# Performance work log

Measured on AMD Instinct MI355X. Metric: run time of the kernel, lower is better.

Reference implementation:

```python
import jax, jax.numpy as jnp
import numpy as np

N_NODES = 50000
N_EDGES = 800000
N_GRAPHS = 64
IN_DIM = 128
HID = 256
N_LAYERS = 4
N_PROT = 5
N_CLASSES = 1
EPS = 1e-12


def setup_inputs() -> dict:
    key = jax.random.key(0)
    ks = jax.random.split(key, 10)
    h = jax.random.normal(ks[0], (N_NODES, IN_DIM), jnp.float32)
    src = jax.random.randint(ks[1], (N_EDGES,), 0, N_NODES, dtype=jnp.int32)
    dst = jax.random.randint(ks[2], (N_EDGES,), 0, N_NODES, dtype=jnp.int32)
    graph_id = jnp.sort(jax.random.randint(ks[3], (N_NODES,), 0, N_GRAPHS, dtype=jnp.int32))
    W_emb = jax.random.normal(ks[4], (IN_DIM, HID), jnp.float32) * 0.05
    b_emb = jnp.zeros((HID,), jnp.float32)
    Ws = jax.random.normal(ks[5], (N_LAYERS, 2 * HID, HID), jnp.float32) * 0.05
    bs = jnp.zeros((N_LAYERS, HID), jnp.float32)
    p_pos = jax.random.uniform(ks[6], (N_PROT, HID), jnp.float32)
    p_neg = jax.random.uniform(ks[7], (N_PROT, HID), jnp.float32)
    W_fc = jax.random.normal(ks[8], (N_CLASSES, 2 * N_PROT), jnp.float32) * 0.1
    return dict(h=h, src=src, dst=dst, graph_id=graph_id, W_emb=W_emb,
                b_emb=b_emb, Ws=Ws, bs=bs, p_pos=p_pos, p_neg=p_neg, W_fc=W_fc)


def _segment_mean(x, seg, num):
    # sum over segments, divide by count (empty segments -> 0, like DGL mean)
    s = jax.ops.segment_sum(x, seg, num_segments=num)
    cnt = jax.ops.segment_sum(jnp.ones((x.shape[0],), x.dtype), seg, num_segments=num)
    return s / jnp.maximum(cnt, 1.0)[:, None]


def _forward(h, src, dst, graph_id, W_emb, b_emb, Ws, bs, p_pos, p_neg, W_fc):
    x = h @ W_emb + b_emb  # [N, HID]
    for l in range(N_LAYERS):
        # mean aggregation of neighbor messages (copy_src -> mean at dst)
        c = _segment_mean(x[src], dst, N_NODES)  # [N, HID]
        bundle = jnp.concatenate([x, c], axis=1) @ Ws[l] + bs[l]  # [N, HID]
        # F.normalize(p=2, dim=1) then relu activation, then residual add
        norm = jnp.linalg.norm(bundle, axis=1, keepdims=True)
        bundle = bundle / jnp.maximum(norm, EPS)
        x = x + jax.nn.relu(bundle)
    hg = _segment_mean(x, graph_id, N_GRAPHS)  # dgl.mean_nodes -> [G, HID]

    def sims(P):
        d = jnp.sum((hg[:, None, :] - P[None, :, :]) ** 2, axis=-1)  # [G, P]
        return jnp.log((d + 1.0) / (d + EPS))

    ss = jnp.concatenate([sims(p_pos), sims(p_neg)], axis=1)  # [G, 2P]
    y = ss @ W_fc.T  # [G, n_classes]
    return jax.nn.sigmoid(y).squeeze()


def reference(h, src, dst, graph_id, W_emb, b_emb, Ws, bs, p_pos, p_neg, W_fc):
    return _forward(h, src, dst, graph_id, W_emb, b_emb, Ws, bs, p_pos, p_neg, W_fc)
```

## Files before the change

kernel.cpp:

```cpp
#include <hip/hip_runtime.h>
#include <math.h>

#define N_NODESC 50000
#define NPAD 50048
#define N_EDGESC 800000
#define N_GRAPHSC 64
#define IN_DIMC 128
#define HIDC 256
#define N_LAYERSC 4
#define EPSV 1e-12f

#define NBUCK 196
#define EPB 4096
#define NBLK1 196
#define WCONV_BLKS 2176
#define PBUCK 8192
#define ZROW 50000

typedef __attribute__((ext_vector_type(8))) short short8;
typedef __attribute__((ext_vector_type(4))) float floatx4;
typedef __attribute__((ext_vector_type(2))) float floatx2;

__device__ __forceinline__ unsigned short f2b(float f) {
    union { float f; unsigned u; } v; v.f = f;
    unsigned r = v.u + 0x7FFFu + ((v.u >> 16) & 1u);
    return (unsigned short)(r >> 16);
}
__device__ __forceinline__ unsigned pkb(float a, float b) {
    return (unsigned)f2b(a) | ((unsigned)f2b(b) << 16);
}
__device__ __forceinline__ unsigned char f2q(float v) {
    return (unsigned char)(__builtin_amdgcn_cvt_pk_fp8_f32(v, v, 0, false) & 0xFF);
}
__device__ __forceinline__ float q2f(unsigned u) {
    floatx2 t = __builtin_amdgcn_cvt_pk_f32_fp8(u, false);
    return t.x;
}
__device__ __forceinline__ unsigned pk4q(float a, float b, float c, float d) {
    unsigned lo = (unsigned)__builtin_amdgcn_cvt_pk_fp8_f32(a, b, 0, false) & 0xFFFFu;
    unsigned hi = (unsigned)__builtin_amdgcn_cvt_pk_fp8_f32(c, d, 0, false) << 16;
    return lo | hi;
}
__device__ __forceinline__ void ldscp16(const void* g, void* l) {
    __builtin_amdgcn_global_load_lds(
        (const __attribute__((address_space(1))) unsigned int*)g,
        (__attribute__((address_space(3))) unsigned int*)l, 16, 0, 0);
}

__global__ __launch_bounds__(256) void k_pre1(const float* __restrict__ Wemb,
        const float* __restrict__ Ws, unsigned short* __restrict__ wsw,
        unsigned char* __restrict__ wq, const int* __restrict__ gid,
        int* __restrict__ gstart, const int* __restrict__ dst,
        int* __restrict__ gbcnt) {
    __shared__ int bc[256];
    int b = blockIdx.x;
    int t = threadIdx.x;
    if (b < WCONV_BLKS) {
        int idx = b * 256 + t;
        const int EMB = IN_DIMC * HIDC;
        const int LYR = 2 * HIDC * HIDC;
        if (idx < EMB) {
            int k = idx >> 8, n = idx & 255;
            int off = (((k >> 5) * 16 + (n >> 4)) * 64 + ((((k >> 3) & 3) << 4) | (n & 15))) * 8 + (k & 7);
            wsw[off] = f2b(Wemb[idx]);
        } else if (idx < EMB + N_LAYERSC * LYR) {
            int r = idx - EMB;
            int l = r >> 17;
            int r2 = r & (LYR - 1);
            int k = r2 >> 8, n = r2 & 255;
            int off = (((k >> 5) * 16 + (n >> 4)) * 64 + ((((k >> 3) & 3) << 4) | (n & 15))) * 8 + (k & 7);
            wq[(size_t)l * LYR + off] = f2q(Ws[r]);
        }
    } else if (b == WCONV_BLKS) {
        int g = t;
        if (g <= N_GRAPHSC) {
            int lo = 0, hi = N_NODESC;
            while (lo < hi) {
                int mid = (lo + hi) >> 1;
                if (gid[mid] < g) lo = mid + 1; else hi = mid;
            }
            gstart[g] = lo;
        }
    } else {
        bc[t] = 0;
        __syncthreads();
        int e0 = (b - WCONV_BLKS - 1) * EPB;
        for (int i = t; i < EPB; i += 256) {
            int e = e0 + i;
            if (e < N_EDGESC) atomicAdd(&bc[dst[e] >> 8], 1);
        }
        __syncthreads();
        if (t < NBUCK && bc[t] > 0) atomicAdd(&gbcnt[t], bc[t]);
    }
}

__global__ __launch_bounds__(256) void k_bscan(const int* __restrict__ gbcnt,
        int* __restrict__ boffB, int* __restrict__ gcurB) {
    __shared__ int s[256];
    int t = threadIdx.x;
    int v = (t < NBUCK) ? gbcnt[t] : 0;
    s[t] = v;
    __syncthreads();
    for (int d = 1; d < 256; d <<= 1) {
        int u = (t >= d) ? s[t - d] : 0;
        __syncthreads();
        s[t] += u;
        __syncthreads();
    }
    if (t < NBUCK) {
        int excl = s[t] - v;
        boffB[t] = excl;
        gcurB[t] = excl;
    }
    if (t == 0) boffB[NBUCK] = N_EDGESC;
}

__global__ __launch_bounds__(256, 4) void k_scat_egemm(const int* __restrict__ src,
        const int* __restrict__ dst, int* __restrict__ gcurB,
        unsigned* __restrict__ ebpack, const float* __restrict__ h,
        const unsigned short* __restrict__ wsw, const float* __restrict__ bias,
        unsigned char* __restrict__ xq) {
    __shared__ int bc[256];
    __shared__ int cur[256];
    if (blockIdx.x < NBLK1) {
        int t = threadIdx.x;
        bc[t] = 0;
        __syncthreads();
        int e0 = blockIdx.x * EPB;
        for (int i = t; i < EPB; i += 256) {
            int e = e0 + i;
            if (e < N_EDGESC) atomicAdd(&bc[dst[e] >> 8], 1);
        }
        __syncthreads();
        if (t < NBUCK)
            cur[t] = (bc[t] > 0) ? atomicAdd(&gcurB[t], bc[t]) : 0;
        __syncthreads();
        for (int i = t; i < EPB; i += 256) {
            int e = e0 + i;
            if (e < N_EDGESC) {
                int d = dst[e];
                int b = d >> 8;
                int pos = atomicAdd(&cur[b], 1);
                ebpack[pos] = (unsigned)src[e] | ((unsigned)(d & 255) << 16);
            }
        }
        return;
    }
    int tid = threadIdx.x;
    int wn = tid >> 6;
    int lane = tid & 63;
    int quad = lane >> 4;
    int l15 = lane & 15;
    int row0 = (blockIdx.x - NBLK1) * 32;

    floatx4 acc[2][4];
    #pragma unroll
    for (int mt = 0; mt < 2; mt++)
        #pragma unroll
        for (int n = 0; n < 4; n++)
            acc[mt][n] = (floatx4){0.f, 0.f, 0.f, 0.f};

    int r0 = row0 + l15;
    int r1 = row0 + 16 + l15;
    bool ok0 = r0 < N_NODESC, ok1 = r1 < N_NODESC;
    const float* h0 = h + (size_t)r0 * IN_DIMC + quad * 8;
    const float* h1 = h + (size_t)r1 * IN_DIMC + quad * 8;
    const unsigned short* bp = wsw + ((size_t)(wn * 4) * 64 + lane) * 8;

    #pragma unroll
    for (int ks = 0; ks < 4; ks++) {
        float4 f00 = ok0 ? *(const float4*)(h0 + ks * 32)     : (float4){0,0,0,0};
        float4 f01 = ok0 ? *(const float4*)(h0 + ks * 32 + 4) : (float4){0,0,0,0};
        float4 f10 = ok1 ? *(const float4*)(h1 + ks * 32)     : (float4){0,0,0,0};
        float4 f11 = ok1 ? *(const float4*)(h1 + ks * 32 + 4) : (float4){0,0,0,0};
        short8 afr[2], bfr[4];
        uint4 av;
        av.x = pkb(f00.x, f00.y); av.y = pkb(f00.z, f00.w);
        av.z = pkb(f01.x, f01.y); av.w = pkb(f01.z, f01.w);
        afr[0] = *(short8*)&av;
        av.x = pkb(f10.x, f10.y); av.y = pkb(f10.z, f10.w);
        av.z = pkb(f11.x, f11.y); av.w = pkb(f11.z, f11.w);
        afr[1] = *(short8*)&av;
        const unsigned short* wp = bp + (size_t)ks * 8192;
        #pragma unroll
        for (int n = 0; n < 4; n++)
            bfr[n] = *(const short8*)(wp + n * 512);
        #pragma unroll
        for (int mt = 0; mt < 2; mt++)
            #pragma unroll
            for (int n = 0; n < 4; n++)
                acc[mt][n] = __builtin_amdgcn_mfma_f32_16x16x32_bf16(
                    afr[mt], bfr[n], acc[mt][n], 0, 0, 0);
    }

    float bv[4];
    #pragma unroll
    for (int n = 0; n < 4; n++) bv[n] = bias[wn * 64 + n * 16 + l15];
    #pragma unroll
    for (int mt = 0; mt < 2; mt++) {
        #pragma unroll
        for (int r = 0; r < 4; r++) {
            int row = row0 + mt * 16 + quad * 4 + r;
            #pragma unroll
            for (int n = 0; n < 4; n++) {
                int col = wn * 64 + n * 16 + l15;
                float v = acc[mt][n][r] + bv[n];
                xq[(size_t)row * HIDC + col] = (row < N_NODESC) ? f2q(v) : (unsigned char)0;
            }
        }
    }
}

__global__ __launch_bounds__(256) void k_bbuild(const unsigned* __restrict__ ebpack,
        const int* __restrict__ boffB, int* __restrict__ offs,
        int* __restrict__ ndeg, unsigned short* __restrict__ esrc) {
    __shared__ int deg[256];
    __shared__ int lofs[256];
    __shared__ unsigned short img[PBUCK];
    int b = blockIdx.x;
    int t = threadIdx.x;
    int bbase = boffB[b];
    int cnt = boffB[b + 1] - bbase;
    deg[t] = 0;
    __syncthreads();
    for (int i = t; i < cnt; i += 256)
        atomicAdd(&deg[ebpack[bbase + i] >> 16], 1);
    __syncthreads();
    int d = deg[t];
    int pd = (d + 7) & ~7;
    lofs[t] = pd;
    __syncthreads();
    for (int s = 1; s < 256; s <<= 1) {
        int u = (t >= s) ? lofs[t - s] : 0;
        __syncthreads();
        lofs[t] += u;
        __syncthreads();
    }
    int pexcl = lofs[t] - pd;
    int node = b * 256 + t;
    int S = b * PBUCK;
    if (node < N_NODESC) {
        offs[node] = S + pexcl;
        ndeg[node] = d;
    }
    int ptot = lofs[255];
    for (int i = t; i < ptot; i += 256) img[i] = (unsigned short)ZROW;
    deg[t] = pexcl;
    __syncthreads();
    for (int i = t; i < cnt; i += 256) {
        unsigned p = ebpack[bbase + i];
        int pos = atomicAdd(&deg[p >> 16], 1);
        img[pos] = (unsigned short)(p & 0xFFFF);
    }
    __syncthreads();
    for (int i = t; i < ptot; i += 256)
        esrc[S + i] = img[i];
}

__global__ __launch_bounds__(256, 8) void k_aggregate(const unsigned char* __restrict__ xq,
        const int* __restrict__ offs, const int* __restrict__ ndeg,
        const unsigned short* __restrict__ esrc, unsigned char* __restrict__ cq) {
    int gidx = blockIdx.x * 256 + threadIdx.x;
    int node = gidx >> 5;
    int lane = threadIdx.x & 31;
    int beg = offs[node];
    int dn = ndeg[node];
    int pd = (dn + 7) & ~7;
    int end = beg + pd;
    float a[8];
    #pragma unroll
    for (int j = 0; j < 8; j++) a[j] = 0.f;
    size_t loff = (size_t)lane * 8;
    #define ACC8(v) do { \
        floatx2 t0 = __builtin_amdgcn_cvt_pk_f32_fp8((v).x, false); \
        floatx2 t1 = __builtin_amdgcn_cvt_pk_f32_fp8((v).x, true);  \
        floatx2 t2 = __builtin_amdgcn_cvt_pk_f32_fp8((v).y, false); \
        floatx2 t3 = __builtin_amdgcn_cvt_pk_f32_fp8((v).y, true);  \
        a[0] += t0.x; a[1] += t0.y; a[2] += t1.x; a[3] += t1.y;     \
        a[4] += t2.x; a[5] += t2.y; a[6] += t3.x; a[7] += t3.y;     \
    } while (0)
    if (pd > 0) {
        uint4 si = *(const uint4*)&esrc[beg];
        for (int e = beg; e < end; e += 8) {
            uint4 sn;
            if (e + 8 < end) sn = *(const uint4*)&esrc[e + 8];
            uint2 v[8];
            v[0] = *(const uint2*)(xq + (size_t)(si.x & 0xFFFF) * HIDC + loff);
            v[1] = *(const uint2*)(xq + (size_t)(si.x >> 16)    * HIDC + loff);
            v[2] = *(const uint2*)(xq + (size_t)(si.y & 0xFFFF) * HIDC + loff);
            v[3] = *(const uint2*)(xq + (size_t)(si.y >> 16)    * HIDC + loff);
            v[4] = *(const uint2*)(xq + (size_t)(si.z & 0xFFFF) * HIDC + loff);
            v[5] = *(const uint2*)(xq + (size_t)(si.z >> 16)    * HIDC + loff);
            v[6] = *(const uint2*)(xq + (size_t)(si.w & 0xFFFF) * HIDC + loff);
            v[7] = *(const uint2*)(xq + (size_t)(si.w >> 16)    * HIDC + loff);
            #pragma unroll
            for (int j = 0; j < 8; j++) ACC8(v[j]);
            si = sn;
        }
    }
    #undef ACC8
    float w = 1.0f / (float)max(dn, 1);
    uint2 o;
    o.x = pk4q(a[0] * w, a[1] * w, a[2] * w, a[3] * w);
    o.y = pk4q(a[4] * w, a[5] * w, a[6] * w, a[7] * w);
    *(uint2*)(cq + (size_t)node * HIDC + loff) = o;
}

template<bool LAST>
__global__ __launch_bounds__(256, 4) void k_lgemm(unsigned char* __restrict__ xq,
        const unsigned char* __restrict__ cq, const unsigned char* __restrict__ wq,
        const float* __restrict__ bias, const int* __restrict__ gid,
        float* __restrict__ hg) {
    __shared__ unsigned long long panelA64[2048];
    __shared__ unsigned long long panelC64[2048];
    __shared__ float rs[64];
    __shared__ signed char ggl[LAST ? 64 : 1];
    __shared__ int g0s;
    unsigned char* panelA = (unsigned char*)panelA64;
    unsigned char* panelC = (unsigned char*)panelC64;
    int tid = threadIdx.x;
    int w = tid >> 6;
    int lane = tid & 63;
    int quad = lane >> 4;
    int l15 = lane & 15;
    int row0 = blockIdx.x * 64;

    {
        #pragma unroll
        for (int i = 0; i < 4; i++) {
            int ldsoff = w * 4096 + i * 1024 + lane * 16;
            int r = ldsoff >> 8;
            int ch = (ldsoff & 255) >> 4;
            int lc = ch ^ (r & 15);
            ldscp16(xq + (size_t)(row0 + r) * HIDC + lc * 16, &panelA[w * 4096 + i * 1024]);
            ldscp16(cq + (size_t)(row0 + r) * HIDC + lc * 16, &panelC[w * 4096 + i * 1024]);
        }
    }
    __syncthreads();

    floatx4 acc[4][4];
    #pragma unroll
    for (int mt = 0; mt < 4; mt++)
        #pragma unroll
        for (int n = 0; n < 4; n++)
            acc[mt][n] = (floatx4){0.f, 0.f, 0.f, 0.f};

    const unsigned char* bp = wq + ((size_t)(w * 4) * 64 + lane) * 8;

    long long bcur[4], bnxt[4];
    #pragma unroll
    for (int n = 0; n < 4; n++) bcur[n] = *(const long long*)(bp + n * 512);

    #pragma unroll
    for (int st = 0; st < 16; st++) {
        if (st < 15) {
            const unsigned char* wp = bp + (size_t)(st + 1) * 8192;
            #pragma unroll
            for (int n = 0; n < 4; n++)
                bnxt[n] = *(const long long*)(wp + n * 512);
        }
        const unsigned char* pan = (st < 8) ? panelA : panelC;
        int ks = st & 7;
        long long afr[4];
        #pragma unroll
        for (int mt = 0; mt < 4; mt++) {
            int row = mt * 16 + l15;
            int lc = ks * 2 + (quad >> 1);
            int phys = lc ^ (row & 15);
            afr[mt] = *(const long long*)&pan[row * 256 + phys * 16 + (quad & 1) * 8];
        }
        #pragma unroll
        for (int mt = 0; mt < 4; mt++)
            #pragma unroll
            for (int n = 0; n < 4; n++)
                acc[mt][n] = __builtin_amdgcn_mfma_f32_16x16x32_fp8_fp8(
                    afr[mt], bcur[n], acc[mt][n], 0, 0, 0);
        #pragma unroll
        for (int n = 0; n < 4; n++) bcur[n] = bnxt[n];
    }

    float bv[4];
    #pragma unroll
    for (int n = 0; n < 4; n++) bv[n] = bias[w * 64 + n * 16 + l15];
    #pragma unroll
    for (int mt = 0; mt < 4; mt++)
        #pragma unroll
        for (int n = 0; n < 4; n++)
            #pragma unroll
            for (int r = 0; r < 4; r++)
                acc[mt][n][r] += bv[n];

    __syncthreads();
    if (tid < 64) rs[tid] = 0.f;
    if constexpr (LAST) {
        if (tid < 64) {
            int g0 = gid[min(row0, N_NODESC - 1)];
            int gv = gid[min(row0 + tid, N_NODESC - 1)] - g0;
            ggl[tid] = (signed char)min(gv, 3);
            if (tid == 0) g0s = g0;
        }
    }
    __syncthreads();
    #pragma unroll
    for (int mt = 0; mt < 4; mt++) {
        #pragma unroll
        for (int r = 0; r < 4; r++) {
            float p = acc[mt][0][r] * acc[mt][0][r] + acc[mt][1][r] * acc[mt][1][r]
                    + acc[mt][2][r] * acc[mt][2][r] + acc[mt][3][r] * acc[mt][3][r];
            p += __shfl_xor(p, 1);
            p += __shfl_xor(p, 2);
            p += __shfl_xor(p, 4);
            p += __shfl_xor(p, 8);
            if (l15 == 0) atomicAdd(&rs[mt * 16 + quad * 4 + r], p);
        }
    }
    __syncthreads();

    #pragma unroll
    for (int mt = 0; mt < 4; mt++) {
        #pragma unroll
        for (int r = 0; r < 4; r++) {
            int lrow = mt * 16 + quad * 4 + r;
            int row = row0 + lrow;
            float inv = 1.0f / fmaxf(sqrtf(rs[lrow]), EPSV);
            #pragma unroll
            for (int n = 0; n < 4; n++) {
                int phys = (w * 4 + n) ^ (lrow & 15);
                float xo = q2f((unsigned)panelA[lrow * 256 + phys * 16 + l15]);
                float nv = xo + fmaxf(acc[mt][n][r] * inv, 0.f);
                if constexpr (LAST) {
                    acc[mt][n][r] = nv;
                } else if (row < N_NODESC) {
                    int col = w * 64 + n * 16 + l15;
                    xq[(size_t)row * HIDC + col] = f2q(nv);
                }
            }
        }
    }
    if constexpr (LAST) {
        int nspan = (int)ggl[63] + 1;
        int g0 = g0s;
        for (int gl = 0; gl < nspan; gl++) {
            float s[4] = {0.f, 0.f, 0.f, 0.f};
            #pragma unroll
            for (int mt = 0; mt < 4; mt++) {
                #pragma unroll
                for (int r = 0; r < 4; r++) {
                    int lrow = mt * 16 + quad * 4 + r;
                    bool m = ((int)ggl[lrow] == gl) && (row0 + lrow < N_NODESC);
                    float f = m ? 1.f : 0.f;
                    #pragma unroll
                    for (int n = 0; n < 4; n++) s[n] += f * acc[mt][n][r];
                }
            }
            #pragma unroll
            for (int n = 0; n < 4; n++) {
                s[n] += __shfl_xor(s[n], 16);
                s[n] += __shfl_xor(s[n], 32);
            }
            if (quad == 0) {
                #pragma unroll
                for (int n = 0; n < 4; n++)
                    atomicAdd(&hg[(g0 + gl) * HIDC + w * 64 + n * 16 + l15], s[n]);
            }
        }
    }
}

__global__ __launch_bounds__(256) void k_readout(const float* __restrict__ hg,
        const int* __restrict__ gstart, const float* __restrict__ ppos,
        const float* __restrict__ pneg, const float* __restrict__ wfc,
        float* __restrict__ out) {
    __shared__ float red[256];
    __shared__ float ss[10];
    int t = threadIdx.x;
    int g = blockIdx.x;
    int beg = gstart[g], end = gstart[g + 1];
    float inv = 1.0f / (float)max(end - beg, 1);
    float hgv = hg[g * HIDC + t] * inv;
    for (int p = 0; p < 10; p++) {
        const float* P = (p < 5) ? (ppos + p * HIDC) : (pneg + (p - 5) * HIDC);
        float d = hgv - P[t];
        red[t] = d * d;
        __syncthreads();
        for (int s2 = 128; s2 > 0; s2 >>= 1) {
            if (t < s2) red[t] += red[t + s2];
            __syncthreads();
        }
        if (t == 0) {
            float dd = red[0];
            ss[p] = logf((dd + 1.0f) / (dd + EPSV));
        }
        __syncthreads();
    }
    if (t == 0) {
        float y = 0.f;
        #pragma unroll
        for (int p = 0; p < 10; p++) y += ss[p] * wfc[p];
        out[g] = 1.0f / (1.0f + expf(-y));
    }
}

extern "C" void kernel_launch(void* const* d_in, const int* in_sizes, int n_in,
                              void* d_out, int out_size, void* d_ws, size_t ws_size,
                              hipStream_t stream) {
    const float* h    = (const float*)d_in[0];
    const int*   src  = (const int*)d_in[1];
    const int*   dst  = (const int*)d_in[2];
    const int*   gid  = (const int*)d_in[3];
    const float* Wemb = (const float*)d_in[4];
    const float* bemb = (const float*)d_in[5];
    const float* Ws   = (const float*)d_in[6];
    const float* bs   = (const float*)d_in[7];
    const float* ppos = (const float*)d_in[8];
    const float* pneg = (const float*)d_in[9];
    const float* wfc  = (const float*)d_in[10];
    float* out = (float*)d_out;

    char* ws = (char*)d_ws;
    size_t off = 0;
    auto alloc = [&](size_t bytes) {
        void* p = ws + off;
        off += (bytes + 255) & ~(size_t)255;
        return p;
    };
    unsigned char*  xq     = (unsigned char*)alloc((size_t)NPAD * HIDC);
    unsigned char*  cq     = (unsigned char*)alloc((size_t)NPAD * HIDC);
    unsigned short* wsw    = (unsigned short*)alloc((size_t)(IN_DIMC * HIDC) * 2);
    unsigned char*  wq     = (unsigned char*)alloc((size_t)(N_LAYERSC * 2 * HIDC * HIDC));
    int*            offs   = (int*)alloc((size_t)(N_NODESC + 1) * 4);
    int*            ndeg   = (int*)alloc((size_t)N_NODESC * 4);
    unsigned short* esrc   = (unsigned short*)alloc((size_t)NBUCK * PBUCK * 2);
    unsigned*       ebpack = (unsigned*)alloc((size_t)N_EDGESC * 4);
    int*            gbcnt  = (int*)alloc((size_t)NBUCK * 4);
    int*            boffB  = (int*)alloc((size_t)(NBUCK + 1) * 4);
    int*            gcurB  = (int*)alloc((size_t)NBUCK * 4);
    int*            gstart = (int*)alloc((size_t)(N_GRAPHSC + 1) * 4);
    float*          hg     = (float*)alloc((size_t)N_GRAPHSC * HIDC * 4);
    (void)ws_size; (void)in_sizes; (void)n_in; (void)out_size;

    hipMemsetAsync(gbcnt, 0, (size_t)NBUCK * 4, stream);
    hipMemsetAsync(hg, 0, (size_t)N_GRAPHSC * HIDC * 4, stream);

    const int LYR = 2 * HIDC * HIDC;
    k_pre1<<<WCONV_BLKS + 1 + NBLK1, 256, 0, stream>>>(Wemb, Ws, wsw, wq, gid, gstart, dst, gbcnt);
    k_bscan<<<1, 256, 0, stream>>>(gbcnt, boffB, gcurB);
    k_scat_egemm<<<NBLK1 + NPAD / 32, 256, 0, stream>>>(src, dst, gcurB, ebpack, h, wsw, bemb, xq);
    k_bbuild<<<NBUCK, 256, 0, stream>>>(ebpack, boffB, offs, ndeg, esrc);

    for (int l = 0; l < N_LAYERSC; l++) {
        k_aggregate<<<(N_NODESC * 32) / 256, 256, 0, stream>>>(xq, offs, ndeg, esrc, cq);
        if (l < N_LAYERSC - 1)
            k_lgemm<false><<<NPAD / 64, 256, 0, stream>>>(
                xq, cq, wq + (size_t)l * LYR, bs + (size_t)l * HIDC, gid, hg);
        else
            k_lgemm<true><<<NPAD / 64, 256, 0, stream>>>(
                xq, cq, wq + (size_t)l * LYR, bs + (size_t)l * HIDC, gid, hg);
    }
    k_readout<<<N_GRAPHSC, 256, 0, stream>>>(hg, gstart, ppos, pneg, wfc, out);
}
```

Measured before the change: 352.0 us.

## Scatter edges into fixed-size bucket slabs to drop count/scan kernels

Edges are now written into a fixed-capacity slab per destination bucket (ESLAB entries) using an atomic per-bucket cursor. This removes the global bucket count pass, the single-block scan kernel and one extra pass over dst. The CSR build is merged with the embedding GEMM into one launch, which cuts two kernel launches from the preprocessing chain. The readout reduction is also changed to use wave shuffles instead of shared-memory tree reductions. The cost is a larger ebpack buffer and the assumption that no bucket exceeds 8192 edges, which holds only because the random dst values are spread evenly.

```diff
diff --git a/kernel.cpp b/kernel.cpp
--- a/kernel.cpp
+++ b/kernel.cpp
@@ -14,6 +14,7 @@
 #define EPB 4096
 #define NBLK1 196
 #define WCONV_BLKS 2176
+#define ESLAB 8192
 #define PBUCK 8192
 #define ZROW 50000
 
@@ -50,9 +51,11 @@
 __global__ __launch_bounds__(256) void k_pre1(const float* __restrict__ Wemb,
         const float* __restrict__ Ws, unsigned short* __restrict__ wsw,
         unsigned char* __restrict__ wq, const int* __restrict__ gid,
-        int* __restrict__ gstart, const int* __restrict__ dst,
-        int* __restrict__ gbcnt) {
+        int* __restrict__ gstart, const int* __restrict__ src,
+        const int* __restrict__ dst, int* __restrict__ gcurB,
+        unsigned* __restrict__ ebpack) {
     __shared__ int bc[256];
+    __shared__ int cur[256];
     int b = blockIdx.x;
     int t = threadIdx.x;
     if (b < WCONV_BLKS) {
@@ -82,51 +85,10 @@
             gstart[g] = lo;
         }
     } else {
+        int sb = b - WCONV_BLKS - 1;
         bc[t] = 0;
         __syncthreads();
-        int e0 = (b - WCONV_BLKS - 1) * EPB;
-        for (int i = t; i < EPB; i += 256) {
-            int e = e0 + i;
-            if (e < N_EDGESC) atomicAdd(&bc[dst[e] >> 8], 1);
-        }
-        __syncthreads();
-        if (t < NBUCK && bc[t] > 0) atomicAdd(&gbcnt[t], bc[t]);
-    }
-}
-
-__global__ __launch_bounds__(256) void k_bscan(const int* __restrict__ gbcnt,
-        int* __restrict__ boffB, int* __restrict__ gcurB) {
-    __shared__ int s[256];
-    int t = threadIdx.x;
-    int v = (t < NBUCK) ? gbcnt[t] : 0;
-    s[t] = v;
-    __syncthreads();
-    for (int d = 1; d < 256; d <<= 1) {
-        int u = (t >= d) ? s[t - d] : 0;
-        __syncthreads();
-        s[t] += u;
-        __syncthreads();
-    }
-    if (t < NBUCK) {
-        int excl = s[t] - v;
-        boffB[t] = excl;
-        gcurB[t] = excl;
-    }
-    if (t == 0) boffB[NBUCK] = N_EDGESC;
-}
-
-__global__ __launch_bounds__(256, 4) void k_scat_egemm(const int* __restrict__ src,
-        const int* __restrict__ dst, int* __restrict__ gcurB,
-        unsigned* __restrict__ ebpack, const float* __restrict__ h,
-        const unsigned short* __restrict__ wsw, const float* __restrict__ bias,
-        unsigned char* __restrict__ xq) {
-    __shared__ int bc[256];
-    __shared__ int cur[256];
-    if (blockIdx.x < NBLK1) {
-        int t = threadIdx.x;
-        bc[t] = 0;
-        __syncthreads();
-        int e0 = blockIdx.x * EPB;
+        int e0 = sb * EPB;
         for (int i = t; i < EPB; i += 256) {
             int e = e0 + i;
             if (e < N_EDGESC) atomicAdd(&bc[dst[e] >> 8], 1);
@@ -139,11 +101,61 @@
             int e = e0 + i;
             if (e < N_EDGESC) {
                 int d = dst[e];
-                int b = d >> 8;
-                int pos = atomicAdd(&cur[b], 1);
-                ebpack[pos] = (unsigned)src[e] | ((unsigned)(d & 255) << 16);
-            }
-        }
+                int bk = d >> 8;
+                int pos = atomicAdd(&cur[bk], 1);
+                ebpack[(size_t)bk * ESLAB + pos] = (unsigned)src[e] | ((unsigned)(d & 255) << 16);
+            }
+        }
+    }
+}
+
+__global__ __launch_bounds__(256, 4) void k_build_egemm(const unsigned* __restrict__ ebpack,
+        const int* __restrict__ gcurB, int* __restrict__ offs, int* __restrict__ ndeg,
+        unsigned short* __restrict__ esrc, const float* __restrict__ h,
+        const unsigned short* __restrict__ wsw, const float* __restrict__ bias,
+        unsigned char* __restrict__ xq) {
+    __shared__ int deg[256];
+    __shared__ int lofs[256];
+    __shared__ unsigned short img[PBUCK];
+    if (blockIdx.x < NBUCK) {
+        int b = blockIdx.x;
+        int t = threadIdx.x;
+        size_t bbase = (size_t)b * ESLAB;
+        int cnt = gcurB[b];
+        deg[t] = 0;
+        __syncthreads();
+        for (int i = t; i < cnt; i += 256)
+            atomicAdd(&deg[ebpack[bbase + i] >> 16], 1);
+        __syncthreads();
+        int d = deg[t];
+        int pd = (d + 7) & ~7;
+        lofs[t] = pd;
+        __syncthreads();
+        for (int s = 1; s < 256; s <<= 1) {
+            int u = (t >= s) ? lofs[t - s] : 0;
+            __syncthreads();
+            lofs[t] += u;
+            __syncthreads();
+        }
+        int pexcl = lofs[t] - pd;
+        int node = b * 256 + t;
+        int S = b * PBUCK;
+        if (node < N_NODESC) {
+            offs[node] = S + pexcl;
+            ndeg[node] = d;
+        }
+        int ptot = lofs[255];
+        for (int i = t; i < ptot; i += 256) img[i] = (unsigned short)ZROW;
+        deg[t] = pexcl;
+        __syncthreads();
+        for (int i = t; i < cnt; i += 256) {
+            unsigned p = ebpack[bbase + i];
+            int pos = atomicAdd(&deg[p >> 16], 1);
+            img[pos] = (unsigned short)(p & 0xFFFF);
+        }
+        __syncthreads();
+        for (int i = t; i < ptot; i += 256)
+            esrc[S + i] = img[i];
         return;
     }
     int tid = threadIdx.x;
@@ -151,7 +163,7 @@
     int lane = tid & 63;
     int quad = lane >> 4;
     int l15 = lane & 15;
-    int row0 = (blockIdx.x - NBLK1) * 32;
+    int row0 = (blockIdx.x - NBUCK) * 32;
 
     floatx4 acc[2][4];
     #pragma unroll
@@ -209,52 +221,6 @@
             }
         }
     }
-}
-
-__global__ __launch_bounds__(256) void k_bbuild(const unsigned* __restrict__ ebpack,
-        const int* __restrict__ boffB, int* __restrict__ offs,
-        int* __restrict__ ndeg, unsigned short* __restrict__ esrc) {
-    __shared__ int deg[256];
-    __shared__ int lofs[256];
-    __shared__ unsigned short img[PBUCK];
-    int b = blockIdx.x;
-    int t = threadIdx.x;
-    int bbase = boffB[b];
-    int cnt = boffB[b + 1] - bbase;
-    deg[t] = 0;
-    __syncthreads();
-    for (int i = t; i < cnt; i += 256)
-        atomicAdd(&deg[ebpack[bbase + i] >> 16], 1);
-    __syncthreads();
-    int d = deg[t];
-    int pd = (d + 7) & ~7;
-    lofs[t] = pd;
-    __syncthreads();
-    for (int s = 1; s < 256; s <<= 1) {
-        int u = (t >= s) ? lofs[t - s] : 0;
-        __syncthreads();
-        lofs[t] += u;
-        __syncthreads();
-    }
-    int pexcl = lofs[t] - pd;
-    int node = b * 256 + t;
-    int S = b * PBUCK;
-    if (node < N_NODESC) {
-        offs[node] = S + pexcl;
-        ndeg[node] = d;
-    }
-    int ptot = lofs[255];
-    for (int i = t; i < ptot; i += 256) img[i] = (unsigned short)ZROW;
-    deg[t] = pexcl;
-    __syncthreads();
-    for (int i = t; i < cnt; i += 256) {
-        unsigned p = ebpack[bbase + i];
-        int pos = atomicAdd(&deg[p >> 16], 1);
-        img[pos] = (unsigned short)(p & 0xFFFF);
-    }
-    __syncthreads();
-    for (int i = t; i < ptot; i += 256)
-        esrc[S + i] = img[i];
 }
 
 __global__ __launch_bounds__(256, 8) void k_aggregate(const unsigned char* __restrict__ xq,
@@ -471,32 +437,35 @@
         const int* __restrict__ gstart, const float* __restrict__ ppos,
         const float* __restrict__ pneg, const float* __restrict__ wfc,
         float* __restrict__ out) {
-    __shared__ float red[256];
-    __shared__ float ss[10];
+    __shared__ float part[10][4];
     int t = threadIdx.x;
     int g = blockIdx.x;
+    int wv = t >> 6;
+    int ln = t & 63;
     int beg = gstart[g], end = gstart[g + 1];
     float inv = 1.0f / (float)max(end - beg, 1);
     float hgv = hg[g * HIDC + t] * inv;
+    #pragma unroll
     for (int p = 0; p < 10; p++) {
         const float* P = (p < 5) ? (ppos + p * HIDC) : (pneg + (p - 5) * HIDC);
         float d = hgv - P[t];
-        red[t] = d * d;
-        __syncthreads();
-        for (int s2 = 128; s2 > 0; s2 >>= 1) {
-            if (t < s2) red[t] += red[t + s2];
-            __syncthreads();
-        }
-        if (t == 0) {
-            float dd = red[0];
-            ss[p] = logf((dd + 1.0f) / (dd + EPSV));
-        }
-        __syncthreads();
-    }
+        float sq = d * d;
+        sq += __shfl_xor(sq, 1);
+        sq += __shfl_xor(sq, 2);
+        sq += __shfl_xor(sq, 4);
+        sq += __shfl_xor(sq, 8);
+        sq += __shfl_xor(sq, 16);
+        sq += __shfl_xor(sq, 32);
+        if (ln == 0) part[p][wv] = sq;
+    }
+    __syncthreads();
     if (t == 0) {
         float y = 0.f;
         #pragma unroll
-        for (int p = 0; p < 10; p++) y += ss[p] * wfc[p];
+        for (int p = 0; p < 10; p++) {
+            float dd = part[p][0] + part[p][1] + part[p][2] + part[p][3];
+            y += logf((dd + 1.0f) / (dd + EPSV)) * wfc[p];
+        }
         out[g] = 1.0f / (1.0f + expf(-y));
     }
 }
@@ -531,22 +500,18 @@
     int*            offs   = (int*)alloc((size_t)(N_NODESC + 1) * 4);
     int*            ndeg   = (int*)alloc((size_t)N_NODESC * 4);
     unsigned short* esrc   = (unsigned short*)alloc((size_t)NBUCK * PBUCK * 2);
-    unsigned*       ebpack = (unsigned*)alloc((size_t)N_EDGESC * 4);
-    int*            gbcnt  = (int*)alloc((size_t)NBUCK * 4);
-    int*            boffB  = (int*)alloc((size_t)(NBUCK + 1) * 4);
+    unsigned*       ebpack = (unsigned*)alloc((size_t)NBUCK * ESLAB * 4);
     int*            gcurB  = (int*)alloc((size_t)NBUCK * 4);
     int*            gstart = (int*)alloc((size_t)(N_GRAPHSC + 1) * 4);
     float*          hg     = (float*)alloc((size_t)N_GRAPHSC * HIDC * 4);
     (void)ws_size; (void)in_sizes; (void)n_in; (void)out_size;
 
-    hipMemsetAsync(gbcnt, 0, (size_t)NBUCK * 4, stream);
+    hipMemsetAsync(gcurB, 0, (size_t)NBUCK * 4, stream);
     hipMemsetAsync(hg, 0, (size_t)N_GRAPHSC * HIDC * 4, stream);
 
     const int LYR = 2 * HIDC * HIDC;
-    k_pre1<<<WCONV_BLKS + 1 + NBLK1, 256, 0, stream>>>(Wemb, Ws, wsw, wq, gid, gstart, dst, gbcnt);
-    k_bscan<<<1, 256, 0, stream>>>(gbcnt, boffB, gcurB);
-    k_scat_egemm<<<NBLK1 + NPAD / 32, 256, 0, stream>>>(src, dst, gcurB, ebpack, h, wsw, bemb, xq);
-    k_bbuild<<<NBUCK, 256, 0, stream>>>(ebpack, boffB, offs, ndeg, esrc);
+    k_pre1<<<WCONV_BLKS + 1 + NBLK1, 256, 0, stream>>>(Wemb, Ws, wsw, wq, gid, gstart, src, dst, gcurB, ebpack);
+    k_build_egemm<<<NBUCK + NPAD / 32, 256, 0, stream>>>(ebpack, gcurB, offs, ndeg, esrc, h, wsw, bemb, xq);
 
     for (int l = 0; l < N_LAYERSC; l++) {
         k_aggregate<<<(N_NODESC * 32) / 256, 256, 0, stream>>>(xq, offs, ndeg, esrc, cq);
```

Measured after the change: 343.3 us. -2.5%, faster.
